# Kernel optimization log

Measured on AMD Instinct MI355X. Metric: run time of the kernel, lower is better.

## Reference

```python
import jax, jax.numpy as jnp
import numpy as np

B, S, H, L = 64, 512, 1024, 9


def setup_inputs() -> dict:
    key = jax.random.key(0)
    k1, k2, k3, k4 = jax.random.split(key, 4)
    sequence_output = jax.random.normal(k1, (B, S, H), dtype=jnp.float32)
    valid_mask = jax.random.randint(k2, (B, S), 0, 2, dtype=jnp.int32)
    # classifier params (Dense(num_labels), TruncatedNormal(stddev=0.02) ~ normal here)
    W = jax.random.normal(k3, (H, L), dtype=jnp.float32) * 0.02
    b = jnp.zeros((L,), dtype=jnp.float32)
    return {"sequence_output": sequence_output, "valid_mask": valid_mask, "W": W, "b": b}


def _compact_valid(sequence_output, valid_mask):
    # Stable-sort tokens so valid (mask==1) tokens come first in original order,
    # then zero-pad the tail -- vectorized equivalent of the per-token Python loop.
    Bq, Sq, _ = sequence_output.shape
    pos = jnp.arange(Sq, dtype=jnp.int32)[None, :]                 # [1,S]
    sort_key = (1 - valid_mask) * Sq + pos                         # invalid pushed back, stable
    order = jnp.argsort(sort_key, axis=1)                          # [B,S]
    gathered = jnp.take_along_axis(sequence_output, order[:, :, None], axis=1)
    n_valid = jnp.sum(valid_mask, axis=1, keepdims=True)           # [B,1]
    keep = (pos < n_valid)[:, :, None]                             # [B,S,1]
    return jnp.where(keep, gathered, jnp.zeros((), sequence_output.dtype))


def reference(sequence_output, valid_mask, W, b):
    valid_output = _compact_valid(sequence_output, valid_mask)     # [B,S,H]
    # dropout is identity at inference (training=False)
    logits = jnp.einsum("bsh,hl->bsl", valid_output, W) + b
    return jax.nn.softmax(logits, axis=-1)
```

## Files before the change

### kernel.cpp

```cpp
#include <hip/hip_runtime.h>
#include <hip/hip_bf16.h>

#define BB 64
#define SS 512
#define HH 1024
#define LL 9

template <int CTRL>
__device__ __forceinline__ float dpp_add(float v) {
    int s = __builtin_bit_cast(int, v);
    int r = __builtin_amdgcn_update_dpp(0, s, CTRL, 0xF, 0xF, true);
    return v + __builtin_bit_cast(float, r);
}

__global__ __launch_bounds__(256, 2) void fused_ner_kernel(
    const float* __restrict__ x, const int* __restrict__ mask,
    const float* __restrict__ W, const float* __restrict__ bias,
    float* __restrict__ out) {
    __shared__ __align__(16) float Wl[HH * LL];
    __shared__ int gidx_sh[SS];
    __shared__ int wsum[4];
    __shared__ float bsh[LL];
    __shared__ float obuf[64 * LL];

    const int tid  = threadIdx.x;
    const int bat  = blockIdx.x & 63;
    const int blk  = blockIdx.x >> 6;
    const int lane = tid & 63;
    const int wv_  = tid >> 6;

    #pragma unroll
    for (int i = 0; i < 9; ++i) {
        const int f4 = i * 256 + tid;
        __builtin_amdgcn_global_load_lds(
            (const __attribute__((address_space(1))) void*)(W + f4 * 4),
            (__attribute__((address_space(3))) void*)(&Wl[f4 * 4]),
            16, 0, 0);
    }
    if (tid < LL) bsh[tid] = bias[tid];

    const int2 mm = reinterpret_cast<const int2*>(mask + bat * SS)[tid];
    const int m0 = mm.x, m1 = mm.y;
    const int s = m0 + m1;
    int incl = s;
    #pragma unroll
    for (int off = 1; off < 64; off <<= 1) {
        int u = __shfl_up(incl, off, 64);
        if (lane >= off) incl += u;
    }
    if (lane == 63) wsum[wv_] = incl;
    __syncthreads();
    int wbase = 0;
    #pragma unroll
    for (int i = 0; i < 4; ++i) if (i < wv_) wbase += wsum[i];
    const int nv = wsum[0] + wsum[1] + wsum[2] + wsum[3];
    const int excl = incl - s + wbase;
    if (m0) gidx_sh[excl] = 2 * tid;
    if (m1) gidx_sh[excl + m0] = 2 * tid + 1;
    __syncthreads();

    float wf[4][36];
    #pragma unroll
    for (int i = 0; i < 4; ++i) {
        const float* wp = &Wl[(i * 64 + lane) * 36];
        #pragma unroll
        for (int j = 0; j < 9; ++j) {
            const float4 t = *reinterpret_cast<const float4*>(wp + j * 4);
            wf[i][j * 4 + 0] = t.x;
            wf[i][j * 4 + 1] = t.y;
            wf[i][j * 4 + 2] = t.z;
            wf[i][j * 4 + 3] = t.w;
        }
    }

    const int jbeg = (blk * nv) >> 3;
    const int jend = ((blk + 1) * nv) >> 3;
    const int nwork = jend - jbeg;
    const int npad = SS - nv;
    const int pbeg = nv + ((blk * npad) >> 3);
    const int pend = nv + (((blk + 1) * npad) >> 3);

    #pragma unroll 1
    for (int pass = 0; pass < 8; ++pass) {
        const int lp0 = pass * 8 + wv_ * 2;
        if (lp0 >= nwork) break;

        float sc[2];
        const float4* xr[2];
        #pragma unroll
        for (int r = 0; r < 2; ++r) {
            const int j = jbeg + lp0 + r;
            const bool valid = (j < jend);
            sc[r] = valid ? 1.f : 0.f;
            const int src = gidx_sh[valid ? j : jbeg];
            xr[r] = reinterpret_cast<const float4*>(x + ((size_t)bat * SS + src) * HH);
        }

        float4 xq[2][4];
        #pragma unroll
        for (int i = 0; i < 4; ++i)
            #pragma unroll
            for (int r = 0; r < 2; ++r) xq[r][i] = xr[r][i * 64 + lane];

        float acc[2][LL];
        #pragma unroll
        for (int r = 0; r < 2; ++r)
            #pragma unroll
            for (int l = 0; l < LL; ++l) acc[r][l] = 0.f;

        #pragma unroll
        for (int i = 0; i < 4; ++i) {
            #pragma unroll
            for (int l = 0; l < LL; ++l) {
                #pragma unroll
                for (int r = 0; r < 2; ++r) {
                    const float4 xvv = xq[r][i];
                    acc[r][l] += xvv.x * wf[i][0 * 9 + l] + xvv.y * wf[i][1 * 9 + l]
                               + xvv.z * wf[i][2 * 9 + l] + xvv.w * wf[i][3 * 9 + l];
                }
            }
        }

        #pragma unroll
        for (int r = 0; r < 2; ++r)
            #pragma unroll
            for (int l = 0; l < LL; ++l) {
                float v = acc[r][l];
                v = dpp_add<0x111>(v);
                v = dpp_add<0x112>(v);
                v = dpp_add<0x114>(v);
                v = dpp_add<0x118>(v);
                v = dpp_add<0x142>(v);
                v = dpp_add<0x143>(v);
                acc[r][l] = v;
            }

        if (lane == 63) {
            #pragma unroll
            for (int r = 0; r < 2; ++r) {
                float lg[LL];
                float mx = -3.0e38f;
                #pragma unroll
                for (int l = 0; l < LL; ++l) {
                    lg[l] = acc[r][l] * sc[r] + bsh[l];
                    mx = fmaxf(mx, lg[l]);
                }
                float ssum = 0.f;
                #pragma unroll
                for (int l = 0; l < LL; ++l) { lg[l] = __expf(lg[l] - mx); ssum += lg[l]; }
                const float inv = 1.f / ssum;
                #pragma unroll
                for (int l = 0; l < LL; ++l) obuf[(lp0 + r) * LL + l] = lg[l] * inv;
            }
        }
    }

    float bs[LL];
    float mxb = -3.0e38f;
    #pragma unroll
    for (int l = 0; l < LL; ++l) { bs[l] = bsh[l]; mxb = fmaxf(mxb, bs[l]); }
    float sb = 0.f;
    #pragma unroll
    for (int l = 0; l < LL; ++l) { bs[l] = __expf(bs[l] - mxb); sb += bs[l]; }
    const float invb = 1.f / sb;

    __syncthreads();

    const size_t vbase = ((size_t)bat * SS + jbeg) * LL;
    for (int t = tid; t < nwork * LL; t += 256) out[vbase + t] = obuf[t];

    const size_t pbase = ((size_t)bat * SS + pbeg) * LL;
    const int pn = (pend - pbeg) * LL;
    for (int t = tid; t < pn; t += 256) {
        const int row = t / LL;
        const int l   = t - row * LL;
        out[pbase + t] = bs[l] * invb;
    }
}

extern "C" void kernel_launch(void* const* d_in, const int* in_sizes, int n_in,
                              void* d_out, int out_size, void* d_ws, size_t ws_size,
                              hipStream_t stream) {
    const float* x    = (const float*)d_in[0];
    const int*   mask = (const int*)d_in[1];
    const float* W    = (const float*)d_in[2];
    const float* bias = (const float*)d_in[3];
    float* out = (float*)d_out;

    fused_ner_kernel<<<BB * 8, 256, 0, stream>>>(x, mask, W, bias, out);
}
```

Measured before the change: 22.76 us.

## Read tokens in order and scatter outputs to compacted positions

Gathering valid rows is replaced by a scatter. Each block now reads its 64 consecutive token rows in order and computes logits for every token. Invalid tokens have their dot product scaled by zero, so they yield the bias softmax. A per-token destination index, with the valid flag packed into a bit of a short, routes each output row to its compacted or padded slot. This gives contiguous loads and equal work per block, but it reads every token row, including the roughly half that the old gather path skipped, so HBM traffic for x roughly doubles.

After: 31.83 us. +39.9%, slower.

```diff
diff --git a/kernel.cpp b/kernel.cpp
--- a/kernel.cpp
+++ b/kernel.cpp
@@ -18,14 +18,14 @@
     const float* __restrict__ W, const float* __restrict__ bias,
     float* __restrict__ out) {
     __shared__ __align__(16) float Wl[HH * LL];
-    __shared__ int gidx_sh[SS];
+    __shared__ unsigned short dest_sh[SS];
     __shared__ int wsum[4];
     __shared__ float bsh[LL];
     __shared__ float obuf[64 * LL];
 
     const int tid  = threadIdx.x;
     const int bat  = blockIdx.x & 63;
-    const int blk  = blockIdx.x >> 6;
+    const int seg  = blockIdx.x >> 6;
     const int lane = tid & 63;
     const int wv_  = tid >> 6;
 
@@ -54,9 +54,13 @@
     #pragma unroll
     for (int i = 0; i < 4; ++i) if (i < wv_) wbase += wsum[i];
     const int nv = wsum[0] + wsum[1] + wsum[2] + wsum[3];
-    const int excl = incl - s + wbase;
-    if (m0) gidx_sh[excl] = 2 * tid;
-    if (m1) gidx_sh[excl + m0] = 2 * tid + 1;
+    const int e0 = incl - s + wbase;
+    const int t0g = 2 * tid;
+    const int d0 = m0 ? e0 : nv + (t0g - e0);
+    const int e1 = e0 + m0;
+    const int d1 = m1 ? e1 : nv + (t0g + 1 - e1);
+    dest_sh[t0g]     = (unsigned short)(d0 | (m0 << 15));
+    dest_sh[t0g + 1] = (unsigned short)(d1 | (m1 << 15));
     __syncthreads();
 
     float wf[4][36];
@@ -73,34 +77,21 @@
         }
     }
 
-    const int jbeg = (blk * nv) >> 3;
-    const int jend = ((blk + 1) * nv) >> 3;
-    const int nwork = jend - jbeg;
-    const int npad = SS - nv;
-    const int pbeg = nv + ((blk * npad) >> 3);
-    const int pend = nv + (((blk + 1) * npad) >> 3);
-
     #pragma unroll 1
     for (int pass = 0; pass < 8; ++pass) {
-        const int lp0 = pass * 8 + wv_ * 2;
-        if (lp0 >= nwork) break;
+        const int lt0 = wv_ * 16 + pass * 2;
+        const int t0 = seg * 64 + lt0;
 
-        float sc[2];
-        const float4* xr[2];
-        #pragma unroll
-        for (int r = 0; r < 2; ++r) {
-            const int j = jbeg + lp0 + r;
-            const bool valid = (j < jend);
-            sc[r] = valid ? 1.f : 0.f;
-            const int src = gidx_sh[valid ? j : jbeg];
-            xr[r] = reinterpret_cast<const float4*>(x + ((size_t)bat * SS + src) * HH);
-        }
+        const float4* xr0 = reinterpret_cast<const float4*>(
+            x + ((size_t)bat * SS + t0) * HH);
+        const float4* xr1 = xr0 + (HH / 4);
 
         float4 xq[2][4];
         #pragma unroll
-        for (int i = 0; i < 4; ++i)
-            #pragma unroll
-            for (int r = 0; r < 2; ++r) xq[r][i] = xr[r][i * 64 + lane];
+        for (int i = 0; i < 4; ++i) {
+            xq[0][i] = xr0[i * 64 + lane];
+            xq[1][i] = xr1[i * 64 + lane];
+        }
 
         float acc[2][LL];
         #pragma unroll
@@ -138,11 +129,13 @@
         if (lane == 63) {
             #pragma unroll
             for (int r = 0; r < 2; ++r) {
+                const unsigned short dv = dest_sh[t0 + r];
+                const float sc = (float)(dv >> 15);
                 float lg[LL];
                 float mx = -3.0e38f;
                 #pragma unroll
                 for (int l = 0; l < LL; ++l) {
-                    lg[l] = acc[r][l] * sc[r] + bsh[l];
+                    lg[l] = acc[r][l] * sc + bsh[l];
                     mx = fmaxf(mx, lg[l]);
                 }
                 float ssum = 0.f;
@@ -150,31 +143,19 @@
                 for (int l = 0; l < LL; ++l) { lg[l] = __expf(lg[l] - mx); ssum += lg[l]; }
                 const float inv = 1.f / ssum;
                 #pragma unroll
-                for (int l = 0; l < LL; ++l) obuf[(lp0 + r) * LL + l] = lg[l] * inv;
+                for (int l = 0; l < LL; ++l) obuf[(lt0 + r) * LL + l] = lg[l] * inv;
             }
         }
     }
 
-    float bs[LL];
-    float mxb = -3.0e38f;
-    #pragma unroll
-    for (int l = 0; l < LL; ++l) { bs[l] = bsh[l]; mxb = fmaxf(mxb, bs[l]); }
-    float sb = 0.f;
-    #pragma unroll
-    for (int l = 0; l < LL; ++l) { bs[l] = __expf(bs[l] - mxb); sb += bs[l]; }
-    const float invb = 1.f / sb;
-
     __syncthreads();
 
-    const size_t vbase = ((size_t)bat * SS + jbeg) * LL;
-    for (int t = tid; t < nwork * LL; t += 256) out[vbase + t] = obuf[t];
-
-    const size_t pbase = ((size_t)bat * SS + pbeg) * LL;
-    const int pn = (pend - pbeg) * LL;
-    for (int t = tid; t < pn; t += 256) {
-        const int row = t / LL;
-        const int l   = t - row * LL;
-        out[pbase + t] = bs[l] * invb;
+    const size_t bbase = (size_t)bat * SS * LL;
+    for (int el = tid; el < 64 * LL; el += 256) {
+        const int lt = el / LL;
+        const int l  = el - lt * LL;
+        const int d  = dest_sh[seg * 64 + lt] & 0x1FF;
+        out[bbase + (size_t)d * LL + l] = obuf[el];
     }
 }
 
```
